# Performance work log

Hardware: AMD Instinct MI355X
Metric: run time of the kernel (lower is better)

Reference implementation:

```python
import jax, jax.numpy as jnp
import numpy as np

N, E, E_LBL = 50000, 800000, 200000
D_IN, H = 128, 128


def setup_inputs() -> dict:
    key = jax.random.key(0)
    ks = jax.random.split(key, 12)
    s = 0.05
    return {
        "x": jax.random.normal(ks[0], (N, D_IN), jnp.float32),
        "edge_index": jax.random.randint(ks[1], (2, E), 0, N, jnp.int64),
        "edge_label_index": jax.random.randint(ks[2], (2, E_LBL), 0, N, jnp.int64),
        "pre_w": jax.random.normal(ks[3], (D_IN, H), jnp.float32) * s,
        "pre_b": jax.random.normal(ks[4], (H,), jnp.float32) * s,
        "Wx": jax.random.normal(ks[5], (3, 2, H, H), jnp.float32) * s,  # gates z,r,h x cheb orders T0,T1
        "bx": jax.random.normal(ks[6], (3, H), jnp.float32) * s,
        "Wh": jax.random.normal(ks[7], (3, 2, H, H), jnp.float32) * s,
        "bh": jax.random.normal(ks[8], (3, H), jnp.float32) * s,
        "post_w": jax.random.normal(ks[9], (H, 2), jnp.float32) * s,
        "post_b": jax.random.normal(ks[10], (2,), jnp.float32) * s,
    }


def reference(x, edge_index, edge_label_index, pre_w, pre_b, Wx, bx, Wh, bh, post_w, post_b):
    n = x.shape[0]
    src, dst = edge_index[0], edge_index[1]

    # Scaled Chebyshev Laplacian (sym norm, lambda_max=2): L_hat = -D^{-1/2} A D^{-1/2}
    # (diagonal of L_hat is exactly 0, so only off-diagonal edge terms remain).
    deg = jax.ops.segment_sum(jnp.ones_like(src, dtype=x.dtype), src, num_segments=n)
    dinv = jnp.where(deg > 0, jax.lax.rsqrt(jnp.maximum(deg, 1.0)), 0.0)
    w = -(dinv[src] * dinv[dst])  # [E]

    def lap(v):  # L_hat @ v : gather src rows, weight, scatter-add at dst
        return jax.ops.segment_sum(w[:, None] * v[src], dst, num_segments=n)

    def cheb(v, Lv, W2, b):  # ChebConv K=2: T0(v)@W0 + T1(v)@W1 + b
        return v @ W2[0] + Lv @ W2[1] + b

    # pre: Linear(input_dim -> hidden)
    Xh = x @ pre_w + pre_b  # [N, H]
    LX = lap(Xh)

    # GConvGRU single step, H0 = 0
    Hc = jnp.zeros_like(Xh)
    LH = lap(Hc)
    Z = jax.nn.sigmoid(cheb(Xh, LX, Wx[0], bx[0]) + cheb(Hc, LH, Wh[0], bh[0]))
    R = jax.nn.sigmoid(cheb(Xh, LX, Wx[1], bx[1]) + cheb(Hc, LH, Wh[1], bh[1]))
    HR = Hc * R
    LHR = lap(HR)
    Ht = jnp.tanh(cheb(Xh, LX, Wx[2], bx[2]) + cheb(HR, LHR, Wh[2], bh[2]))
    Hc = Z * Hc + (1.0 - Z) * Ht

    h = jax.nn.relu(Hc)
    # link decoder: gather endpoints, hadamard, Linear(H->2), sum over logits
    hprod = h[edge_label_index[0]] * h[edge_label_index[1]]  # [E_lbl, H]
    out = hprod @ post_w + post_b  # [E_lbl, 2]
    return jnp.sum(out, axis=-1)  # [E_lbl]
```

## Files before the change

### kernel.cpp

```cpp
#include <hip/hip_runtime.h>
#include <math.h>


#define RND 4096
#define SORT_CAP 1536
#define CAPB 6144

typedef __attribute__((ext_vector_type(4))) float f32x4;
typedef __attribute__((ext_vector_type(8))) short short8;

static __device__ __forceinline__ unsigned short f2b(float f) {
  union { float f; unsigned u; } v; v.f = f;
  unsigned r = (v.u + 0x7fffu + ((v.u >> 16) & 1u)) >> 16;
  return (unsigned short)r;
}
static __device__ __forceinline__ float b2f(unsigned short s) {
  union { unsigned u; float f; } v; v.u = ((unsigned)s) << 16;
  return v.f;
}

__global__ __launch_bounds__(256) void prep_kernel(const float* __restrict__ pre_w, const float* __restrict__ Wx,
                                                   const float* __restrict__ bx, const float* __restrict__ bh,
                                                   const float* __restrict__ post_w, const float* __restrict__ post_b,
                                                   unsigned short* __restrict__ Bt1c, unsigned short* __restrict__ Btc2,
                                                   float* __restrict__ fb2, float* __restrict__ pwsum,
                                                   int* __restrict__ deg, int* __restrict__ binPos, int N) {
  int e = blockIdx.x * 256 + threadIdx.x;
  const int TOT = gridDim.x * 256;
  for (int i = e; i < N; i += TOT) deg[i] = 0;
  if (e < 256) binPos[e] = e * CAPB;
  if (e < 16384) {
    int kc = e >> 12, r = e & 4095, col = r >> 5, kk = r & 31;
    Bt1c[e] = f2b(pre_w[(kc * 32 + kk) * 128 + col]);
  }
  int e2 = e - 16384;
  if (e2 >= 0 && e2 < 65536) {
    int kc = e2 >> 13, r = e2 & 8191, cB = r >> 5, kk = r & 31;
    int k = kc * 32 + kk, half = k >> 7, ki = k & 127;
    int cb = cB >> 7, r7 = cB & 127, nw6 = r7 >> 6, u2 = r7 & 63;
    int g = (u2 >= 32) ? 2 : 0, hcol = cb * 64 + nw6 * 32 + (u2 & 31);
    Btc2[e2] = f2b(Wx[((g * 2 + half) * 128 + ki) * 128 + hcol]);
  }
  int e3 = e - (16384 + 65536);
  if (e3 >= 0 && e3 < 256) {
    int cB = e3;
    int cb = cB >> 7, r7 = cB & 127, nw6 = r7 >> 6, u2 = r7 & 63;
    int g = (u2 >= 32) ? 2 : 0, hcol = cb * 64 + nw6 * 32 + (u2 & 31);
    fb2[cB] = bx[g * 128 + hcol] + bh[g * 128 + hcol];
  }
  int e4 = e - (16384 + 65536 + 256);
  if (e4 >= 0 && e4 < 128) pwsum[e4] = post_w[2 * e4] + post_w[2 * e4 + 1];
  if (e4 == 128) pwsum[128] = post_b[0] + post_b[1];
}

union SMemU {
  struct { unsigned short As[128 * 40]; unsigned short Bs[128 * 40]; } g;
  struct { unsigned ent[RND]; int hist[256], scanbuf[256], lstart[256],
           lofs[256], gbase[256]; unsigned char ebin[RND]; } s;
};

__global__ __launch_bounds__(256) void mega1_kernel(const float* __restrict__ x,
                                                    const unsigned short* __restrict__ Bt1c,
                                                    const float* __restrict__ pre_b,
                                                    unsigned short* __restrict__ Xq,
                                                    const int* __restrict__ ei, int* __restrict__ binPos,
                                                    unsigned* __restrict__ bins, int* __restrict__ deg,
                                                    int N, int E, int RB) {
  __shared__ SMemU sm;
  const int t = threadIdx.x;

  if ((int)blockIdx.x < RB) {
    unsigned short* As = sm.g.As;
    unsigned short* Bs = sm.g.Bs;
    const int r0 = blockIdx.x * 128;
    const int w = t >> 6, lane = t & 63;
    const int m = lane & 15, q = lane >> 4;
    const int mw = (w >> 1) * 64, nw = (w & 1) * 64;

    f32x4 acc[4][4];
#pragma unroll
    for (int i = 0; i < 4; ++i)
#pragma unroll
      for (int j = 0; j < 4; ++j) acc[i][j] = {0.f, 0.f, 0.f, 0.f};

    const int arow = t >> 1, aseg = t & 1;
    const bool arow_ok = (r0 + arow) < N;
    const float* asrc0 = &x[(size_t)(r0 + arow) * 128 + aseg * 16];

    float4 cav[4]; short8 cbv0, cbv1;
    {
      if (arow_ok) {
#pragma unroll
        for (int i = 0; i < 4; ++i) cav[i] = *(const float4*)(asrc0 + i * 4);
      } else {
#pragma unroll
        for (int i = 0; i < 4; ++i) cav[i] = make_float4(0.f, 0.f, 0.f, 0.f);
      }
      const char* src = (const char*)Bt1c + t * 32;
      cbv0 = *(const short8*)src;
      cbv1 = *(const short8*)(src + 16);
    }

    for (int kc = 0; kc < 4; ++kc) {
      __syncthreads();
      {
        short8 t0, t1;
#pragma unroll
        for (int i = 0; i < 2; ++i) {
          t0[i * 4 + 0] = (short)f2b(cav[i].x); t0[i * 4 + 1] = (short)f2b(cav[i].y);
          t0[i * 4 + 2] = (short)f2b(cav[i].z); t0[i * 4 + 3] = (short)f2b(cav[i].w);
          t1[i * 4 + 0] = (short)f2b(cav[i + 2].x); t1[i * 4 + 1] = (short)f2b(cav[i + 2].y);
          t1[i * 4 + 2] = (short)f2b(cav[i + 2].z); t1[i * 4 + 3] = (short)f2b(cav[i + 2].w);
        }
        *(short8*)&As[arow * 40 + aseg * 16] = t0;
        *(short8*)&As[arow * 40 + aseg * 16 + 8] = t1;
        int bcol = t >> 1, boff = (t & 1) * 16;
        *(short8*)&Bs[bcol * 40 + boff] = cbv0;
        *(short8*)&Bs[bcol * 40 + boff + 8] = cbv1;
      }
      float4 nav[4]; short8 nbv0, nbv1;
      if (kc < 3) {
        if (arow_ok) {
          const float* src = asrc0 + (kc + 1) * 32;
#pragma unroll
          for (int i = 0; i < 4; ++i) nav[i] = *(const float4*)(src + i * 4);
        } else {
#pragma unroll
          for (int i = 0; i < 4; ++i) nav[i] = make_float4(0.f, 0.f, 0.f, 0.f);
        }
        const char* src = (const char*)Bt1c + (size_t)(kc + 1) * 8192 + t * 32;
        nbv0 = *(const short8*)src;
        nbv1 = *(const short8*)(src + 16);
      }
      __syncthreads();
      short8 af[4], bf[4];
#pragma unroll
      for (int i = 0; i < 4; ++i) af[i] = *(const short8*)&As[(mw + i * 16 + m) * 40 + q * 8];
#pragma unroll
      for (int j = 0; j < 4; ++j) bf[j] = *(const short8*)&Bs[(nw + j * 16 + m) * 40 + q * 8];
#pragma unroll
      for (int i = 0; i < 4; ++i)
#pragma unroll
        for (int j = 0; j < 4; ++j)
          acc[i][j] = __builtin_amdgcn_mfma_f32_16x16x32_bf16(af[i], bf[j], acc[i][j], 0, 0, 0);
      if (kc < 3) {
#pragma unroll
        for (int i = 0; i < 4; ++i) cav[i] = nav[i];
        cbv0 = nbv0; cbv1 = nbv1;
      }
    }

#pragma unroll
    for (int i = 0; i < 4; ++i) {
      int rb2 = r0 + mw + i * 16 + q * 4;
#pragma unroll
      for (int j = 0; j < 4; ++j) {
        int col = nw + j * 16 + m;
        float bias = pre_b[col];
#pragma unroll
        for (int r = 0; r < 4; ++r) {
          int row = rb2 + r;
          if (row < N) Xq[(size_t)row * 128 + col] = f2b(acc[i][j][r] + bias);
        }
      }
    }
    return;
  }

  unsigned* ent = sm.s.ent;
  unsigned char* ebin = sm.s.ebin;
  int* hist = sm.s.hist;
  int* scanbuf = sm.s.scanbuf;
  int* lstart = sm.s.lstart;
  int* lofs = sm.s.lofs;
  int* gbase = sm.s.gbase;
  const int sbid = (int)blockIdx.x - RB;
  const int snum = (int)gridDim.x - RB;
  for (long long base = (long long)sbid * RND; base < E; base += (long long)snum * RND) {
    int cnt = (int)(((long long)E - base < RND) ? (E - base) : RND);
    if (t < 256) hist[t] = 0;
    __syncthreads();
    unsigned my_e[16]; int my_b[16];
#pragma unroll
    for (int u = 0; u < 16; ++u) {
      int i = u * 256 + t;
      my_b[u] = -1;
      if (i < cnt) {
        int idx = (int)base + i;
        int s = ei[idx], d = ei[E + idx];
        atomicAdd(&deg[s], 1);
        my_b[u] = d >> 8;
        my_e[u] = (unsigned)s | ((unsigned)(d & 255) << 16);
        atomicAdd(&hist[my_b[u]], 1);
      }
    }
    __syncthreads();
    scanbuf[t] = hist[t];
    __syncthreads();
    for (int d = 1; d < 256; d <<= 1) {
      int v = (t >= d) ? scanbuf[t - d] : 0;
      __syncthreads();
      scanbuf[t] += v;
      __syncthreads();
    }
    int excl = scanbuf[t] - hist[t];
    lstart[t] = excl;
    lofs[t] = excl;
    if (hist[t] > 0) gbase[t] = atomicAdd(&binPos[t], hist[t]);
    __syncthreads();
#pragma unroll
    for (int u = 0; u < 16; ++u) {
      if (my_b[u] >= 0) {
        int p = atomicAdd(&lofs[my_b[u]], 1);
        ent[p] = my_e[u];
        ebin[p] = (unsigned char)my_b[u];
      }
    }
    __syncthreads();
    for (int i = t; i < cnt; i += 256) {
      int b = ebin[i];
      int pos = gbase[b] + (i - lstart[b]);
      if (pos < (b + 1) * CAPB) bins[pos] = ent[i];
    }
    __syncthreads();
  }
}

__global__ __launch_bounds__(512) void lap_bin_kernel(const unsigned short* __restrict__ Xq,
                                                      unsigned short* __restrict__ LXc,
                                                      const unsigned* __restrict__ bins,
                                                      const int* __restrict__ binPos,
                                                      const int* __restrict__ deg, int N) {
  __shared__ unsigned eLDS[CAPB];
  __shared__ unsigned short sortS[SORT_CAP];
  __shared__ float sortW[SORT_CAP];
  __shared__ int hist[64], start[64], off[64];
  const int t = threadIdx.x;
  const int bin = blockIdx.x >> 2, qt = blockIdx.x & 3;
  const int lo = bin * CAPB;
  int T = binPos[bin] - lo;
  if (T > CAPB) T = CAPB;
  const unsigned* __restrict__ ebase = &bins[lo];
  if (t < 64) hist[t] = 0;
  __syncthreads();
  for (int i = t; i < T; i += 512) {
    unsigned e = ebase[i];
    eLDS[i] = e;
    int dl = (e >> 16) & 255;
    if ((dl >> 6) == qt) atomicAdd(&hist[dl & 63], 1);
  }
  __syncthreads();
  if (t < 64) {
    int h = hist[t];
    int v = h;
#pragma unroll
    for (int d = 1; d < 64; d <<= 1) {
      int u = __shfl_up(v, d);
      if (t >= d) v += u;
    }
    start[t] = v - h;
    off[t] = v - h;
  }
  __syncthreads();
  for (int i = t; i < T; i += 512) {
    unsigned e = eLDS[i];
    int dl = (e >> 16) & 255;
    if ((dl >> 6) == qt) {
      int s = (int)(e & 0xFFFFu);
      int p = atomicAdd(&off[dl & 63], 1);
      if (p < SORT_CAP) {
        int dg = deg[s];
        sortS[p] = (unsigned short)s;
        sortW[p] = dg > 0 ? rsqrtf((float)dg) : 0.0f;
      }
    }
  }
  __syncthreads();
  const int wv = t >> 6, lane = t & 63;
  for (int n = wv; n < 64; n += 8) {
    int node = bin * 256 + qt * 64 + n;
    if (node >= N) break;
    int st = start[n], cnum = hist[n];
    float ax = 0.f, ay = 0.f;
    for (int j = 0; j < cnum; j += 8) {
      unsigned v[8]; float ws[8];
#pragma unroll
      for (int u = 0; u < 8; ++u) {
        int idx = j + u;
        int s = 0; float w = 0.f;
        if (idx < cnum) { s = sortS[st + idx]; w = sortW[st + idx]; }
        ws[u] = w;
        v[u] = *(const unsigned*)((const char*)Xq + (size_t)s * 256 + lane * 4);
      }
#pragma unroll
      for (int u = 0; u < 8; ++u) {
        union { unsigned u32; float f; } fl, fh;
        fl.u32 = v[u] << 16; fh.u32 = v[u] & 0xffff0000u;
        ax += ws[u] * fl.f;
        ay += ws[u] * fh.f;
      }
    }
    int dgn = deg[node];
    float wd = dgn > 0 ? -rsqrtf((float)dgn) : 0.0f;
    unsigned o = (unsigned)f2b(ax * wd) | ((unsigned)f2b(ay * wd) << 16);
    *(unsigned*)((char*)LXc + (size_t)node * 256 + lane * 4) = o;
  }
}

__global__ __launch_bounds__(256) void gemm2_mfma(const unsigned short* __restrict__ Xq,
                                                  const unsigned short* __restrict__ LXc,
                                                  const unsigned short* __restrict__ Btc2,
                                                  const float* __restrict__ fb2,
                                                  unsigned short* __restrict__ hb, int N) {
  __shared__ unsigned short As[128 * 40];
  __shared__ unsigned short Bs[128 * 40];
  const int t = threadIdx.x;
  const int rb = blockIdx.x >> 1, cb = blockIdx.x & 1;
  const int r0 = rb * 128;
  const int w = t >> 6, lane = t & 63;
  const int m = lane & 15, q = lane >> 4;
  const int mw = (w >> 1) * 64, nw = (w & 1) * 64;

  f32x4 acc[4][4];
#pragma unroll
  for (int i = 0; i < 4; ++i)
#pragma unroll
    for (int j = 0; j < 4; ++j) acc[i][j] = {0.f, 0.f, 0.f, 0.f};

  const int arow = t >> 1;
  const int aoff = (t & 1) * 32;
  const char* aXq = (const char*)Xq + (size_t)(r0 + arow) * 256 + aoff;
  const char* aLX = (const char*)LXc + (size_t)(r0 + arow) * 256 + aoff;
  const char* bsrc0 = (const char*)Btc2 + (size_t)cb * 8192 + t * 32;

  short8 cav0, cav1, cbv0, cbv1;
  cav0 = *(const short8*)aXq;
  cav1 = *(const short8*)(aXq + 16);
  cbv0 = *(const short8*)bsrc0;
  cbv1 = *(const short8*)(bsrc0 + 16);

  for (int kc = 0; kc < 8; ++kc) {
    __syncthreads();
    *(short8*)&As[arow * 40 + (aoff >> 1)] = cav0;
    *(short8*)&As[arow * 40 + (aoff >> 1) + 8] = cav1;
    {
      int bcol = t >> 1, boff = (t & 1) * 16;
      *(short8*)&Bs[bcol * 40 + boff] = cbv0;
      *(short8*)&Bs[bcol * 40 + boff + 8] = cbv1;
    }
    short8 nav0, nav1, nbv0, nbv1;
    if (kc < 7) {
      int kn = kc + 1;
      const char* asrc = (kn < 4) ? (aXq + kn * 64) : (aLX + (kn - 4) * 64);
      nav0 = *(const short8*)asrc;
      nav1 = *(const short8*)(asrc + 16);
      const char* bsrc = bsrc0 + (size_t)kn * 16384;
      nbv0 = *(const short8*)bsrc;
      nbv1 = *(const short8*)(bsrc + 16);
    }
    __syncthreads();
    short8 af[4], bf[4];
#pragma unroll
    for (int i = 0; i < 4; ++i) af[i] = *(const short8*)&As[(mw + i * 16 + m) * 40 + q * 8];
#pragma unroll
    for (int j = 0; j < 4; ++j) bf[j] = *(const short8*)&Bs[(nw + j * 16 + m) * 40 + q * 8];
#pragma unroll
    for (int i = 0; i < 4; ++i)
#pragma unroll
      for (int j = 0; j < 4; ++j)
        acc[i][j] = __builtin_amdgcn_mfma_f32_16x16x32_bf16(af[i], bf[j], acc[i][j], 0, 0, 0);
    if (kc < 7) { cav0 = nav0; cav1 = nav1; cbv0 = nbv0; cbv1 = nbv1; }
  }

#pragma unroll
  for (int i = 0; i < 4; ++i) {
    int rbase = r0 + mw + i * 16 + q * 4;
#pragma unroll
    for (int jz = 0; jz < 2; ++jz) {
      int cBz = cb * 128 + nw + jz * 16 + m;
      int hc = cb * 64 + (nw >> 1) + jz * 16 + m;
      float bz = fb2[cBz], bt = fb2[cBz + 32];
#pragma unroll
      for (int r = 0; r < 4; ++r) {
        int row = rbase + r;
        if (row < N) {
          float zp = acc[i][jz][r] + bz;
          float tp = acc[i][jz + 2][r] + bt;
          float zs = 1.0f / (1.0f + __expf(-zp));
          float th = tanhf(tp);
          hb[(size_t)row * 128 + hc] = f2b(fmaxf((1.0f - zs) * th, 0.0f));
        }
      }
    }
  }
}

__global__ __launch_bounds__(256) void decoder_kernel(const unsigned short* __restrict__ hb,
                                                      const int* __restrict__ eli,
                                                      const float* __restrict__ pwsum, float* __restrict__ out, int M) {
  int t = threadIdx.x;
  int i = blockIdx.x * 16 + (t >> 4);
  int l = t & 15;
  if (i >= M) return;
  int a = eli[i], b = eli[M + i];
  int k = l * 8;
  short8 va = *(const short8*)&hb[(size_t)a * 128 + k];
  short8 vb = *(const short8*)&hb[(size_t)b * 128 + k];
  const float4* pwp = (const float4*)&pwsum[k];
  float4 p0 = pwp[0], p1 = pwp[1];
  float s = 0.0f;
  s += b2f((unsigned short)va[0]) * b2f((unsigned short)vb[0]) * p0.x;
  s += b2f((unsigned short)va[1]) * b2f((unsigned short)vb[1]) * p0.y;
  s += b2f((unsigned short)va[2]) * b2f((unsigned short)vb[2]) * p0.z;
  s += b2f((unsigned short)va[3]) * b2f((unsigned short)vb[3]) * p0.w;
  s += b2f((unsigned short)va[4]) * b2f((unsigned short)vb[4]) * p1.x;
  s += b2f((unsigned short)va[5]) * b2f((unsigned short)vb[5]) * p1.y;
  s += b2f((unsigned short)va[6]) * b2f((unsigned short)vb[6]) * p1.z;
  s += b2f((unsigned short)va[7]) * b2f((unsigned short)vb[7]) * p1.w;
#pragma unroll
  for (int off = 8; off; off >>= 1) s += __shfl_xor(s, off);
  if (l == 0) out[i] = s + pwsum[128];
}

extern "C" void kernel_launch(void* const* d_in, const int* in_sizes, int n_in,
                              void* d_out, int out_size, void* d_ws, size_t ws_size,
                              hipStream_t stream) {
  const float* x      = (const float*)d_in[0];
  const int*   ei     = (const int*)d_in[1];
  const int*   eli    = (const int*)d_in[2];
  const float* pre_w  = (const float*)d_in[3];
  const float* pre_b  = (const float*)d_in[4];
  const float* Wx     = (const float*)d_in[5];
  const float* bx     = (const float*)d_in[6];
  const float* bh     = (const float*)d_in[8];
  const float* post_w = (const float*)d_in[9];
  const float* post_b = (const float*)d_in[10];
  float* out = (float*)d_out;

  const int N = in_sizes[0] / 128;
  const int E = in_sizes[1] / 2;
  const int M = in_sizes[2] / 2;
  const int RB = (N + 127) / 128;
  const int NBIN = (N + 255) / 256;
  const int SCAT = (E + RND - 1) / RND;

  char* W = (char*)d_ws;
  size_t o = 0;
  int* deg = (int*)(W + o);       o += (size_t)N * 4;
  int* binPos = (int*)(W + o);    o += 1024;
  o = (o + 255) & ~(size_t)255;
  unsigned* bins = (unsigned*)(W + o); o += (size_t)NBIN * CAPB * 4;
  o = (o + 255) & ~(size_t)255;
  unsigned short* Xq = (unsigned short*)(W + o);  o += (size_t)RB * 128 * 256;
  unsigned short* LXc = (unsigned short*)(W + o); o += (size_t)RB * 128 * 256;
  unsigned short* hb = (unsigned short*)(W + o);  o += (size_t)N * 256;
  unsigned short* Bt1c = (unsigned short*)(W + o); o += 32768;
  unsigned short* Btc2 = (unsigned short*)(W + o); o += 131072;
  float* fb2 = (float*)(W + o);  o += 1024;
  float* pwsum = (float*)(W + o); o += 768;

  prep_kernel<<<322, 256, 0, stream>>>(pre_w, Wx, bx, bh, post_w, post_b, Bt1c, Btc2, fb2, pwsum,
                                       deg, binPos, N);
  mega1_kernel<<<RB + SCAT, 256, 0, stream>>>(x, Bt1c, pre_b, Xq, ei, binPos, bins, deg, N, E, RB);
  lap_bin_kernel<<<NBIN * 4, 512, 0, stream>>>(Xq, LXc, bins, binPos, deg, N);
  gemm2_mfma<<<RB * 2, 256, 0, stream>>>(Xq, LXc, Btc2, fb2, hb, N);
  decoder_kernel<<<(M + 15) / 16, 256, 0, stream>>>(hb, eli, pwsum, out, M);
}
```

Measured before the change: 210.1 us.

## Replace global degree atomics with source-binned counts and per-bin LDS histogram

Stops doing one global atomicAdd per edge into deg. Instead, each scatter block also bins edges by source node, writing the low byte of the source index into a new byte array. A new deghist kernel then counts degrees per 256-node bin in LDS and writes deg directly, so deg no longer needs zeroing in prep. The chunk size per scatter block is halved and the 256-entry block scan becomes a wave-shuffle scan. The cost is a second scatter pass, extra bytes written and read, and one more kernel launch.

```diff
diff --git a/kernel.cpp b/kernel.cpp
--- a/kernel.cpp
+++ b/kernel.cpp
@@ -2,7 +2,7 @@
 #include <math.h>
 
 
-#define RND 4096
+#define RND 2048
 #define SORT_CAP 1536
 #define CAPB 6144
 
@@ -24,11 +24,9 @@
                                                    const float* __restrict__ post_w, const float* __restrict__ post_b,
                                                    unsigned short* __restrict__ Bt1c, unsigned short* __restrict__ Btc2,
                                                    float* __restrict__ fb2, float* __restrict__ pwsum,
-                                                   int* __restrict__ deg, int* __restrict__ binPos, int N) {
+                                                   int* __restrict__ binPos) {
   int e = blockIdx.x * 256 + threadIdx.x;
-  const int TOT = gridDim.x * 256;
-  for (int i = e; i < N; i += TOT) deg[i] = 0;
-  if (e < 256) binPos[e] = e * CAPB;
+  if (e < 512) binPos[e] = (e & 255) * CAPB;
   if (e < 16384) {
     int kc = e >> 12, r = e & 4095, col = r >> 5, kk = r & 31;
     Bt1c[e] = f2b(pre_w[(kc * 32 + kk) * 128 + col]);
@@ -55,8 +53,8 @@
 
 union SMemU {
   struct { unsigned short As[128 * 40]; unsigned short Bs[128 * 40]; } g;
-  struct { unsigned ent[RND]; int hist[256], scanbuf[256], lstart[256],
-           lofs[256], gbase[256]; unsigned char ebin[RND]; } s;
+  struct { unsigned ent[RND]; int hist[256], lstart[256], lofs[256], gbase[256], wsum[4];
+           unsigned char ebin[RND], sb[RND]; } s;
 };
 
 __global__ __launch_bounds__(256) void mega1_kernel(const float* __restrict__ x,
@@ -64,7 +62,8 @@
                                                     const float* __restrict__ pre_b,
                                                     unsigned short* __restrict__ Xq,
                                                     const int* __restrict__ ei, int* __restrict__ binPos,
-                                                    unsigned* __restrict__ bins, int* __restrict__ deg,
+                                                    unsigned* __restrict__ bins,
+                                                    unsigned char* __restrict__ sbins,
                                                     int N, int E, int RB) {
   __shared__ SMemU sm;
   const int t = threadIdx.x;
@@ -169,51 +168,56 @@
 
   unsigned* ent = sm.s.ent;
   unsigned char* ebin = sm.s.ebin;
+  unsigned char* sb = sm.s.sb;
   int* hist = sm.s.hist;
-  int* scanbuf = sm.s.scanbuf;
   int* lstart = sm.s.lstart;
   int* lofs = sm.s.lofs;
   int* gbase = sm.s.gbase;
+  int* wsum = sm.s.wsum;
   const int sbid = (int)blockIdx.x - RB;
   const int snum = (int)gridDim.x - RB;
+  const int w = t >> 6, lane = t & 63;
   for (long long base = (long long)sbid * RND; base < E; base += (long long)snum * RND) {
     int cnt = (int)(((long long)E - base < RND) ? (E - base) : RND);
     if (t < 256) hist[t] = 0;
     __syncthreads();
-    unsigned my_e[16]; int my_b[16];
-#pragma unroll
-    for (int u = 0; u < 16; ++u) {
+    int my_s[8], my_d[8];
+#pragma unroll
+    for (int u = 0; u < 8; ++u) {
       int i = u * 256 + t;
-      my_b[u] = -1;
+      my_s[u] = -1;
       if (i < cnt) {
         int idx = (int)base + i;
-        int s = ei[idx], d = ei[E + idx];
-        atomicAdd(&deg[s], 1);
-        my_b[u] = d >> 8;
-        my_e[u] = (unsigned)s | ((unsigned)(d & 255) << 16);
-        atomicAdd(&hist[my_b[u]], 1);
-      }
-    }
-    __syncthreads();
-    scanbuf[t] = hist[t];
-    __syncthreads();
-    for (int d = 1; d < 256; d <<= 1) {
-      int v = (t >= d) ? scanbuf[t - d] : 0;
+        my_s[u] = ei[idx];
+        my_d[u] = ei[E + idx];
+        atomicAdd(&hist[my_d[u] >> 8], 1);
+      }
+    }
+    __syncthreads();
+    {
+      int h = hist[t];
+      hist[t] = 0;
+      int v = h;
+#pragma unroll
+      for (int dd = 1; dd < 64; dd <<= 1) { int uu = __shfl_up(v, dd); if (lane >= dd) v += uu; }
+      if (lane == 63) wsum[w] = v;
       __syncthreads();
-      scanbuf[t] += v;
-      __syncthreads();
-    }
-    int excl = scanbuf[t] - hist[t];
-    lstart[t] = excl;
-    lofs[t] = excl;
-    if (hist[t] > 0) gbase[t] = atomicAdd(&binPos[t], hist[t]);
-    __syncthreads();
-#pragma unroll
-    for (int u = 0; u < 16; ++u) {
-      if (my_b[u] >= 0) {
-        int p = atomicAdd(&lofs[my_b[u]], 1);
-        ent[p] = my_e[u];
-        ebin[p] = (unsigned char)my_b[u];
+      int woff = 0;
+#pragma unroll
+      for (int ww = 0; ww < 3; ++ww) if (ww < w) woff += wsum[ww];
+      int excl = v - h + woff;
+      lstart[t] = excl; lofs[t] = excl;
+      if (h > 0) gbase[t] = atomicAdd(&binPos[t], h);
+    }
+    __syncthreads();
+#pragma unroll
+    for (int u = 0; u < 8; ++u) {
+      if (my_s[u] >= 0) {
+        int b = my_d[u] >> 8;
+        int p = atomicAdd(&lofs[b], 1);
+        ent[p] = (unsigned)my_s[u] | ((unsigned)(my_d[u] & 255) << 16);
+        ebin[p] = (unsigned char)b;
+        atomicAdd(&hist[my_s[u] >> 8], 1);
       }
     }
     __syncthreads();
@@ -223,7 +227,55 @@
       if (pos < (b + 1) * CAPB) bins[pos] = ent[i];
     }
     __syncthreads();
-  }
+    {
+      int h = hist[t];
+      int v = h;
+#pragma unroll
+      for (int dd = 1; dd < 64; dd <<= 1) { int uu = __shfl_up(v, dd); if (lane >= dd) v += uu; }
+      if (lane == 63) wsum[w] = v;
+      __syncthreads();
+      int woff = 0;
+#pragma unroll
+      for (int ww = 0; ww < 3; ++ww) if (ww < w) woff += wsum[ww];
+      int excl = v - h + woff;
+      lstart[t] = excl; lofs[t] = excl;
+      if (h > 0) gbase[t] = atomicAdd(&binPos[256 + t], h);
+    }
+    __syncthreads();
+#pragma unroll
+    for (int u = 0; u < 8; ++u) {
+      if (my_s[u] >= 0) {
+        int b = my_s[u] >> 8;
+        int p = atomicAdd(&lofs[b], 1);
+        sb[p] = (unsigned char)(my_s[u] & 255);
+        ebin[p] = (unsigned char)b;
+      }
+    }
+    __syncthreads();
+    for (int i = t; i < cnt; i += 256) {
+      int b = ebin[i];
+      int pos = gbase[b] + (i - lstart[b]);
+      if (pos < (b + 1) * CAPB) sbins[pos] = sb[i];
+    }
+    __syncthreads();
+  }
+}
+
+__global__ __launch_bounds__(256) void deghist_kernel(const unsigned char* __restrict__ sbins,
+                                                      const int* __restrict__ binPos,
+                                                      int* __restrict__ deg, int N) {
+  __shared__ int h[256];
+  const int t = threadIdx.x;
+  const int bin = blockIdx.x;
+  h[t] = 0;
+  __syncthreads();
+  int T2 = binPos[256 + bin] - bin * CAPB;
+  if (T2 > CAPB) T2 = CAPB;
+  const unsigned char* __restrict__ p = sbins + (size_t)bin * CAPB;
+  for (int i = t; i < T2; i += 256) atomicAdd(&h[p[i]], 1);
+  __syncthreads();
+  int node = bin * 256 + t;
+  if (node < N) deg[node] = h[t];
 }
 
 __global__ __launch_bounds__(512) void lap_bin_kernel(const unsigned short* __restrict__ Xq,
@@ -447,9 +499,11 @@
   char* W = (char*)d_ws;
   size_t o = 0;
   int* deg = (int*)(W + o);       o += (size_t)N * 4;
-  int* binPos = (int*)(W + o);    o += 1024;
+  int* binPos = (int*)(W + o);    o += 2048;
   o = (o + 255) & ~(size_t)255;
   unsigned* bins = (unsigned*)(W + o); o += (size_t)NBIN * CAPB * 4;
+  o = (o + 255) & ~(size_t)255;
+  unsigned char* sbins = (unsigned char*)(W + o); o += (size_t)NBIN * CAPB;
   o = (o + 255) & ~(size_t)255;
   unsigned short* Xq = (unsigned short*)(W + o);  o += (size_t)RB * 128 * 256;
   unsigned short* LXc = (unsigned short*)(W + o); o += (size_t)RB * 128 * 256;
@@ -460,8 +514,9 @@
   float* pwsum = (float*)(W + o); o += 768;
 
   prep_kernel<<<322, 256, 0, stream>>>(pre_w, Wx, bx, bh, post_w, post_b, Bt1c, Btc2, fb2, pwsum,
-                                       deg, binPos, N);
-  mega1_kernel<<<RB + SCAT, 256, 0, stream>>>(x, Bt1c, pre_b, Xq, ei, binPos, bins, deg, N, E, RB);
+                                       binPos);
+  mega1_kernel<<<RB + SCAT, 256, 0, stream>>>(x, Bt1c, pre_b, Xq, ei, binPos, bins, sbins, N, E, RB);
+  deghist_kernel<<<NBIN, 256, 0, stream>>>(sbins, binPos, deg, N);
   lap_bin_kernel<<<NBIN * 4, 512, 0, stream>>>(Xq, LXc, bins, binPos, deg, N);
   gemm2_mfma<<<RB * 2, 256, 0, stream>>>(Xq, LXc, Btc2, fb2, hb, N);
   decoder_kernel<<<(M + 15) / 16, 256, 0, stream>>>(hb, eli, pwsum, out, M);
```

Result: faster. 199.3 us (-5.1%).
